# Kernel optimization log

Hardware: AMD Instinct MI355X
Metric: run time of the kernel (lower is better)

The kernel has to match this reference:

```python
import jax, jax.numpy as jnp
import numpy as np

N = 50000      # nodes
C = 16         # input features
NT = 4         # diffusion scales
K1 = 4         # anisotropic kernels
KEIG = 128     # Laplacian eigenpairs
E = 1600000    # edges
HID = 512
OUT = 256


def setup_inputs() -> dict:
    key = jax.random.key(0)
    ks = jax.random.split(key, 10)
    x = jax.random.normal(ks[0], (N, C), dtype=jnp.float32)
    evals = jax.random.uniform(ks[1], (KEIG,), dtype=jnp.float32)
    evecs = jax.random.normal(ks[2], (N, KEIG), dtype=jnp.float32)
    taus = jax.random.uniform(ks[3], (NT,), dtype=jnp.float32)
    kvals = jax.random.normal(ks[4], (K1, E), dtype=jnp.float32)
    edge_index = jax.random.randint(ks[5], (2, E), 0, N, dtype=jnp.int64)
    W1 = jax.random.normal(ks[6], (C * NT * K1, HID), dtype=jnp.float32) * 0.05
    b1 = jnp.zeros((HID,), dtype=jnp.float32)
    W2 = jax.random.normal(ks[7], (HID, OUT), dtype=jnp.float32) * 0.05
    b2 = jnp.zeros((OUT,), dtype=jnp.float32)
    return {"x": x, "evals": evals, "evecs": evecs, "taus": taus,
            "kvals": kvals, "edge_index": edge_index,
            "W1": W1, "b1": b1, "W2": W2, "b2": b2}


def _diffusion(x, evals, evecs, taus):
    # Spectral heat diffusion at NT learned scales, concatenated on channels.
    coeff = evecs.T @ x                                   # [KEIG, C]
    scales = jnp.exp(-evals[None, :] * taus[:, None])      # [NT, KEIG]
    # [N, NT, C] = evecs @ (scale_t * coeff) per scale
    diff = jnp.einsum('nk,tk,kc->ntc', evecs, scales, coeff)
    return diff.reshape(x.shape[0], -1)                    # [N, NT*C]


def _aniso_conv(x, edge_index, kvals):
    # out_k[i] = sum_{edges j->i} K_k[edge] * x[j]; concat over kernels.
    src, dst = edge_index[0], edge_index[1]
    n = x.shape[0]
    outs = []
    for k in range(kvals.shape[0]):  # small fixed loop over K1 kernels
        msgs = kvals[k][:, None] * x[src]                  # [E, NT*C]
        outs.append(jax.ops.segment_sum(msgs, dst, num_segments=n))
    return jnp.concatenate(outs, axis=-1)                  # [N, K1*NT*C]


def reference(x, evals, evecs, taus, kvals, edge_index, W1, b1, W2, b2):
    h = _diffusion(x, evals, evecs, taus)                  # [N, NT*C]
    h = _aniso_conv(h, edge_index, kvals)                  # [N, K1*NT*C]
    h = jax.nn.relu(h @ W1 + b1)                           # MLP layer 1
    h = h @ W2 + b2                                        # MLP layer 2
    # L2 normalize per node (F.normalize with eps=1e-12)
    nrm = jnp.maximum(jnp.linalg.norm(h, axis=-1, keepdims=True), 1e-12)
    return h / nrm
```

## Files before the change

### kernel.cpp

```cpp
#include <hip/hip_runtime.h>

typedef __bf16 bf16_t;
typedef __attribute__((ext_vector_type(8))) __bf16 bf16x8;
typedef __attribute__((ext_vector_type(4))) float f32x4;
typedef unsigned int uint;
typedef unsigned short ushort;
typedef unsigned char uchar;

#define N_NODES 50000
#define C_IN 16
#define NT 4
#define K1 4
#define KEIG 128
#define E_EDGES 1600000
#define HID 512
#define OUT_F 256
#define FEAT 64
#define CONVF 256
#define M_PAD 50048
#define CPB 1024
#define RED1 64
#define SH_C 8
#define NBC 196
#define CAPC 8704
#define PA_B 782

__device__ inline uint bfbits(float f) {
    bf16_t b = (bf16_t)f;
    return (uint)__builtin_bit_cast(unsigned short, b);
}
__device__ inline float bfu(uint u) {
    return __uint_as_float(u << 16);
}

__global__ void coeff_partial_kernel(const float* __restrict__ evecs,
                                     const float* __restrict__ x,
                                     float* __restrict__ partial,
                                     bf16_t* __restrict__ evb, int n) {
    __shared__ float lds[4 * 2048];
    int t = threadIdx.x, lane = t & 63, wid = t >> 6;
    int gw = blockIdx.x * 4 + wid;
    int total_w = gridDim.x * 4;
    int rpw = (n + total_w - 1) / total_w;
    int r0 = gw * rpw;
    int r1 = min(n, r0 + rpw);
    float acc0[16], acc1[16];
#pragma unroll
    for (int c = 0; c < 16; c++) { acc0[c] = 0.f; acc1[c] = 0.f; }
    for (int r = r0; r < r1; r++) {
        float e0 = evecs[(size_t)r * KEIG + lane];
        float e1 = evecs[(size_t)r * KEIG + 64 + lane];
        evb[(size_t)r * KEIG + lane] = (bf16_t)e0;
        evb[(size_t)r * KEIG + 64 + lane] = (bf16_t)e1;
        const float* xr = &x[(size_t)r * C_IN];
#pragma unroll
        for (int c = 0; c < 16; c++) {
            float xv = xr[c];
            acc0[c] += e0 * xv;
            acc1[c] += e1 * xv;
        }
    }
#pragma unroll
    for (int c = 0; c < 16; c++) {
        lds[wid * 2048 + c * 128 + lane] = acc0[c];
        lds[wid * 2048 + c * 128 + 64 + lane] = acc1[c];
    }
    __syncthreads();
    for (int idx = t; idx < 2048; idx += 256) {
        float s = lds[idx] + lds[2048 + idx] + lds[4096 + idx] + lds[6144 + idx];
        partial[(size_t)blockIdx.x * 2048 + idx] = s;
    }
}

__global__ void coeff_reduce1_kernel(const float* __restrict__ partial,
                                     float* __restrict__ partial2) {
    int g = blockIdx.x >> 3;
    int idx = (blockIdx.x & 7) * 256 + threadIdx.x;
    float s = 0.f;
#pragma unroll
    for (int j = 0; j < 16; j++)
        s += partial[(size_t)(g * 16 + j) * 2048 + idx];
    partial2[(size_t)g * 2048 + idx] = s;
}

__global__ void coeff_reduce2_kernel(const float* __restrict__ partial2,
                                     float* __restrict__ coeff) {
    int idx = blockIdx.x * 256 + threadIdx.x;
    float s = 0.f;
#pragma unroll 8
    for (int b = 0; b < RED1; b++) s += partial2[(size_t)b * 2048 + idx];
    coeff[idx] = s;
}

__global__ void sc2t_kernel(const float* __restrict__ evals,
                            const float* __restrict__ taus,
                            const float* __restrict__ coeff,
                            bf16_t* __restrict__ sc2t) {
    int idx = blockIdx.x * 256 + threadIdx.x;
    int col = idx >> 7, k = idx & 127;
    float v = expf(-evals[k] * taus[col >> 4]) * coeff[(col & 15) * 128 + k];
    sc2t[col * KEIG + k] = (bf16_t)v;
}

#define DSTR 136
__global__ void diffusion_mfma_kernel(const bf16_t* __restrict__ evb,
                                      const bf16_t* __restrict__ sc2t,
                                      bf16_t* __restrict__ diffb) {
    __shared__ bf16_t Alds[128 * DSTR];
    __shared__ bf16_t Blds[64 * DSTR];
    const int t = threadIdx.x;
    const int lane = t & 63;
    const int wid = t >> 6;
    const int row0 = blockIdx.x * 128;
#pragma unroll
    for (int i = 0; i < 8; i++) {
        int idx = t + i * 256;
        int r = idx >> 4;
        int k8 = (idx & 15) * 8;
        *(uint4*)&Alds[r * DSTR + k8] =
            *(const uint4*)&evb[(size_t)(row0 + r) * KEIG + k8];
    }
#pragma unroll
    for (int i = 0; i < 4; i++) {
        int idx = t + i * 256;
        int r = idx >> 4;
        int k8 = (idx & 15) * 8;
        *(uint4*)&Blds[r * DSTR + k8] =
            *(const uint4*)&sc2t[r * KEIG + k8];
    }
    __syncthreads();
    f32x4 acc[2][4];
#pragma unroll
    for (int m = 0; m < 2; m++)
#pragma unroll
        for (int n = 0; n < 4; n++) acc[m][n] = (f32x4){0.f, 0.f, 0.f, 0.f};
#pragma unroll
    for (int kk = 0; kk < 128; kk += 32) {
        int ko = kk + ((lane >> 4) << 3);
        bf16x8 av[2], bv[4];
#pragma unroll
        for (int m = 0; m < 2; m++)
            av[m] = *(const bf16x8*)&Alds[(wid * 32 + m * 16 + (lane & 15)) * DSTR + ko];
#pragma unroll
        for (int n = 0; n < 4; n++)
            bv[n] = *(const bf16x8*)&Blds[(n * 16 + (lane & 15)) * DSTR + ko];
#pragma unroll
        for (int m = 0; m < 2; m++)
#pragma unroll
            for (int n = 0; n < 4; n++)
                acc[m][n] = __builtin_amdgcn_mfma_f32_16x16x32_bf16(
                    av[m], bv[n], acc[m][n], 0, 0, 0);
    }
#pragma unroll
    for (int m = 0; m < 2; m++) {
#pragma unroll
        for (int n = 0; n < 4; n++) {
            int col = n * 16 + (lane & 15);
#pragma unroll
            for (int q = 0; q < 4; q++) {
                int row = row0 + wid * 32 + m * 16 + ((lane >> 4) << 2) + q;
                diffb[(size_t)row * FEAT + col] = (bf16_t)acc[m][n][q];
            }
        }
    }
}

__global__ void radixA_kernel(const int* __restrict__ src,
                              const int* __restrict__ dst,
                              const float* __restrict__ kvals,
                              int* __restrict__ gcursor,
                              int4* __restrict__ bucket, int E) {
    __shared__ int hist[256];
    __shared__ int lds_off[256];
    __shared__ int cnt2[256];
    __shared__ int run_base[256];
    __shared__ int4 recs[2048];
    __shared__ uchar posb[2048];
    int t = threadIdx.x;
    hist[t] = 0; cnt2[t] = 0;
    __syncthreads();
    int e0 = blockIdx.x * 2048;
    int total = min(2048, E - e0);
    int d[8];
#pragma unroll
    for (int j = 0; j < 8; j++) {
        int e = e0 + j * 256 + t;
        d[j] = (e < E) ? dst[e] : -1;
        if (d[j] >= 0) atomicAdd(&hist[d[j] >> SH_C], 1);
    }
    __syncthreads();
    int own = hist[t];
    lds_off[t] = own;
    __syncthreads();
    for (int o = 1; o < 256; o <<= 1) {
        int v = (t >= o) ? lds_off[t - o] : 0;
        __syncthreads();
        lds_off[t] += v;
        __syncthreads();
    }
    int excl = lds_off[t] - own;
    __syncthreads();
    lds_off[t] = excl;
    __syncthreads();
#pragma unroll
    for (int j = 0; j < 8; j++) {
        if (d[j] < 0) continue;
        int e = e0 + j * 256 + t;
        int b = d[j] >> SH_C;
        int r = atomicAdd(&cnt2[b], 1);
        int pos = lds_off[b] + r;
        uint w01 = bfbits(kvals[e]) | (bfbits(kvals[(size_t)E + e]) << 16);
        uint w23 = bfbits(kvals[2 * (size_t)E + e]) | (bfbits(kvals[3 * (size_t)E + e]) << 16);
        int4 rec;
        rec.x = src[e]; rec.y = (int)w01; rec.z = (int)w23; rec.w = d[j] & 255;
        recs[pos] = rec;
        posb[pos] = (uchar)b;
    }
    if (t < NBC) {
        int c = hist[t];
        run_base[t] = c ? atomicAdd(&gcursor[t * 16], c) : 0;
    }
    __syncthreads();
    for (int i = t; i < total; i += 256) {
        int b = posb[i];
        int g = run_base[b] + (i - lds_off[b]);
        if (g < CAPC) bucket[(size_t)b * CAPC + g] = recs[i];
    }
}

__global__ void coarse_scan_kernel(const int* __restrict__ gcursor,
                                   int* __restrict__ coarse_base,
                                   int* __restrict__ row_start) {
    __shared__ int lds[256];
    int t = threadIdx.x;
    int own = (t < NBC) ? min(gcursor[t * 16], CAPC) : 0;
    lds[t] = own;
    __syncthreads();
    for (int o = 1; o < 256; o <<= 1) {
        int v = (t >= o) ? lds[t - o] : 0;
        __syncthreads();
        lds[t] += v;
        __syncthreads();
    }
    if (t < NBC) coarse_base[t] = lds[t] - own;
    if (t == 255) row_start[N_NODES] = lds[255];
}

__global__ void radixB_kernel(const int4* __restrict__ bucket,
                              const int* __restrict__ gcursor,
                              const int* __restrict__ coarse_base,
                              int4* __restrict__ csr_rec,
                              int* __restrict__ row_start) {
    __shared__ int hist[256];
    __shared__ int off[256];
    __shared__ int cnt2[256];
    int b = blockIdx.x, t = threadIdx.x;
    int n = min(gcursor[b * 16], CAPC);
    int base = coarse_base[b];
    hist[t] = 0; cnt2[t] = 0;
    __syncthreads();
    const int4* brec = &bucket[(size_t)b * CAPC];
    for (int i = t; i < n; i += 256) atomicAdd(&hist[brec[i].w & 255], 1);
    __syncthreads();
    int own = hist[t];
    off[t] = own;
    __syncthreads();
    for (int o = 1; o < 256; o <<= 1) {
        int v = (t >= o) ? off[t - o] : 0;
        __syncthreads();
        off[t] += v;
        __syncthreads();
    }
    int excl = off[t] - own;
    __syncthreads();
    off[t] = excl;
    __syncthreads();
    int g = b * 256 + t;
    if (g < N_NODES) row_start[g] = base + off[t];
    for (int i = t; i < n; i += 256) {
        int4 rec = brec[i];
        int w = rec.w & 255;
        int r = atomicAdd(&cnt2[w], 1);
        csr_rec[(size_t)(base + off[w] + r)] = rec;
    }
}

__global__ void aniso_kernel(const bf16_t* __restrict__ diffb_,
                             const int* __restrict__ row_start,
                             const int4* __restrict__ csr_rec,
                             bf16_t* __restrict__ conv, int n) {
    const ushort* diffb = (const ushort*)diffb_;
    int wid = (blockIdx.x * 256 + threadIdx.x) >> 6;
    int lane = threadIdx.x & 63;
    if (wid >= n) return;
    int start = __builtin_amdgcn_readfirstlane(row_start[wid]);
    int end = __builtin_amdgcn_readfirstlane(row_start[wid + 1]);
    float a0 = 0.f, a1 = 0.f, a2 = 0.f, a3 = 0.f;
    int p = start;
    for (; p + 8 <= end; p += 8) {
        int s[8];
        uint wy[8], wz[8];
#pragma unroll
        for (int j = 0; j < 8; j++) {
            int4 rec = csr_rec[p + j];
            s[j] = rec.x; wy[j] = (uint)rec.y; wz[j] = (uint)rec.z;
        }
        float h[8];
#pragma unroll
        for (int j = 0; j < 8; j++)
            h[j] = bfu((uint)diffb[(size_t)s[j] * FEAT + lane]);
#pragma unroll
        for (int j = 0; j < 8; j++) {
            a0 += __uint_as_float(wy[j] << 16) * h[j];
            a1 += __uint_as_float(wy[j] & 0xffff0000u) * h[j];
            a2 += __uint_as_float(wz[j] << 16) * h[j];
            a3 += __uint_as_float(wz[j] & 0xffff0000u) * h[j];
        }
    }
    for (; p < end; p++) {
        int4 rec = csr_rec[p];
        float h0 = bfu((uint)diffb[(size_t)rec.x * FEAT + lane]);
        uint y = (uint)rec.y, z = (uint)rec.z;
        a0 += __uint_as_float(y << 16) * h0;
        a1 += __uint_as_float(y & 0xffff0000u) * h0;
        a2 += __uint_as_float(z << 16) * h0;
        a3 += __uint_as_float(z & 0xffff0000u) * h0;
    }
    size_t base = (size_t)wid * CONVF + lane;
    conv[base]       = (bf16_t)a0;
    conv[base + 64]  = (bf16_t)a1;
    conv[base + 128] = (bf16_t)a2;
    conv[base + 192] = (bf16_t)a3;
}

__global__ void convw_kernel(const float* __restrict__ W, bf16_t* __restrict__ Wt,
                             int rows, int cols) {
    int idx = blockIdx.x * 256 + threadIdx.x;
    if (idx >= rows * cols) return;
    int o = idx / rows, f = idx % rows;
    Wt[idx] = (bf16_t)W[(size_t)f * cols + o];
}

#define BM 128
#define BN 128
#define BK 64
#define LSTR 72

template <int EPI>
__global__ void gemm_bf16_kernel(const bf16_t* __restrict__ A,
                                 const bf16_t* __restrict__ Bt,
                                 const float* __restrict__ bias,
                                 void* __restrict__ Cout,
                                 int Nn, int K, int Mvalid) {
    __shared__ bf16_t Alds[BM * LSTR];
    __shared__ bf16_t Blds[BN * LSTR];
    const int t = threadIdx.x;
    const int lane = t & 63;
    const int wid = t >> 6;
    const int row0 = blockIdx.y * BM;
    const int col0 = blockIdx.x * BN;
    const int wr = (wid >> 1) * 64;
    const int wc = (wid & 1) * 64;

    f32x4 acc[4][4];
#pragma unroll
    for (int m = 0; m < 4; m++)
#pragma unroll
        for (int n = 0; n < 4; n++) acc[m][n] = (f32x4){0.f, 0.f, 0.f, 0.f};

    for (int kt = 0; kt < K; kt += BK) {
#pragma unroll
        for (int i = 0; i < 4; i++) {
            int idx = t + i * 256;
            int r = idx >> 3;
            int k8 = (idx & 7) * 8;
            *(uint4*)&Alds[r * LSTR + k8] =
                *(const uint4*)&A[(size_t)(row0 + r) * K + kt + k8];
            *(uint4*)&Blds[r * LSTR + k8] =
                *(const uint4*)&Bt[(size_t)(col0 + r) * K + kt + k8];
        }
        __syncthreads();
#pragma unroll
        for (int kk = 0; kk < BK; kk += 32) {
            int ko = kk + ((lane >> 4) << 3);
            bf16x8 av[4], bv[4];
#pragma unroll
            for (int m = 0; m < 4; m++)
                av[m] = *(const bf16x8*)&Alds[(wr + m * 16 + (lane & 15)) * LSTR + ko];
#pragma unroll
            for (int n = 0; n < 4; n++)
                bv[n] = *(const bf16x8*)&Blds[(wc + n * 16 + (lane & 15)) * LSTR + ko];
#pragma unroll
            for (int m = 0; m < 4; m++)
#pragma unroll
                for (int n = 0; n < 4; n++)
                    acc[m][n] = __builtin_amdgcn_mfma_f32_16x16x32_bf16(
                        av[m], bv[n], acc[m][n], 0, 0, 0);
        }
        __syncthreads();
    }

#pragma unroll
    for (int n = 0; n < 4; n++) {
        int col = col0 + wc + n * 16 + (lane & 15);
        float bvl = bias[col];
#pragma unroll
        for (int m = 0; m < 4; m++) {
#pragma unroll
            for (int r = 0; r < 4; r++) {
                int row = row0 + wr + m * 16 + ((lane >> 4) << 2) + r;
                float v = acc[m][n][r] + bvl;
                if (EPI == 0) {
                    v = v > 0.f ? v : 0.f;
                    ((bf16_t*)Cout)[(size_t)row * Nn + col] = (bf16_t)v;
                } else {
                    if (row < Mvalid)
                        ((float*)Cout)[(size_t)row * Nn + col] = v;
                }
            }
        }
    }
}

__global__ void norm_kernel(float* __restrict__ out, int n) {
    int w = (blockIdx.x * 256 + threadIdx.x) >> 6;
    int lane = threadIdx.x & 63;
    if (w >= n) return;
    float4 v = *(float4*)&out[(size_t)w * OUT_F + lane * 4];
    float ss = v.x * v.x + v.y * v.y + v.z * v.z + v.w * v.w;
#pragma unroll
    for (int off = 32; off > 0; off >>= 1) ss += __shfl_xor(ss, off);
    float nrm = sqrtf(ss);
    nrm = nrm > 1e-12f ? nrm : 1e-12f;
    float sc = 1.f / nrm;
    v.x *= sc; v.y *= sc; v.z *= sc; v.w *= sc;
    *(float4*)&out[(size_t)w * OUT_F + lane * 4] = v;
}

extern "C" void kernel_launch(void* const* d_in, const int* in_sizes, int n_in,
                              void* d_out, int out_size, void* d_ws, size_t ws_size,
                              hipStream_t stream) {
    const float* x      = (const float*)d_in[0];
    const float* evals  = (const float*)d_in[1];
    const float* evecs  = (const float*)d_in[2];
    const float* taus   = (const float*)d_in[3];
    const float* kvals  = (const float*)d_in[4];
    const int*   eidx   = (const int*)d_in[5];
    const float* W1     = (const float*)d_in[6];
    const float* b1     = (const float*)d_in[7];
    const float* W2     = (const float*)d_in[8];
    const float* b2     = (const float*)d_in[9];
    float* out = (float*)d_out;

    const int N = N_NODES, E = E_EDGES;
    const int* e_src = eidx;
    const int* e_dst = eidx + E;

    char* ws = (char*)d_ws;
    size_t off = 0;
    auto alloc = [&](size_t bytes) {
        void* p = ws + off;
        off = (off + bytes + 255) & ~(size_t)255;
        return p;
    };
    float* coeff       = (float*)alloc(2048 * 4);
    float* partial     = (float*)alloc((size_t)CPB * 2048 * 4);
    float* partial2    = (float*)alloc((size_t)RED1 * 2048 * 4);
    bf16_t* evb        = (bf16_t*)alloc((size_t)M_PAD * KEIG * 2);
    bf16_t* sc2t       = (bf16_t*)alloc((size_t)FEAT * KEIG * 2);
    bf16_t* diffb      = (bf16_t*)alloc((size_t)M_PAD * FEAT * 2);
    int*   gcursor     = (int*)alloc((size_t)NBC * 16 * 4);
    int*   coarse_base = (int*)alloc((size_t)(NBC + 1) * 4);
    int*   row_start   = (int*)alloc((size_t)(N + 1) * 4);
    size_t csr_bytes = (size_t)E * 16;
    size_t h1_bytes  = (size_t)M_PAD * HID * 2;
    int4*  csr_rec   = (int4*)alloc(csr_bytes > h1_bytes ? csr_bytes : h1_bytes);
    bf16_t* h1       = (bf16_t*)csr_rec;
    size_t bucket_bytes = (size_t)NBC * CAPC * 16;
    size_t conv_bytes   = (size_t)M_PAD * CONVF * 2;
    int4*  bucket    = (int4*)alloc(bucket_bytes > conv_bytes ? bucket_bytes : conv_bytes);
    bf16_t* conv     = (bf16_t*)bucket;
    bf16_t* w1t      = (bf16_t*)alloc((size_t)HID * CONVF * 2);
    bf16_t* w2t      = (bf16_t*)alloc((size_t)OUT_F * HID * 2);
    (void)ws_size;

    hipMemsetAsync(gcursor, 0, (size_t)NBC * 16 * 4, stream);

    coeff_partial_kernel<<<CPB, 256, 0, stream>>>(evecs, x, partial, evb, N);
    coeff_reduce1_kernel<<<RED1 * 8, 256, 0, stream>>>(partial, partial2);
    coeff_reduce2_kernel<<<8, 256, 0, stream>>>(partial2, coeff);
    sc2t_kernel<<<32, 256, 0, stream>>>(evals, taus, coeff, sc2t);
    diffusion_mfma_kernel<<<M_PAD / 128, 256, 0, stream>>>(evb, sc2t, diffb);

    radixA_kernel<<<PA_B, 256, 0, stream>>>(e_src, e_dst, kvals, gcursor, bucket, E);
    coarse_scan_kernel<<<1, 256, 0, stream>>>(gcursor, coarse_base, row_start);
    radixB_kernel<<<NBC, 256, 0, stream>>>(bucket, gcursor, coarse_base,
                                           csr_rec, row_start);

    aniso_kernel<<<(N + 3) / 4, 256, 0, stream>>>(diffb, row_start, csr_rec, conv, N);

    convw_kernel<<<(CONVF * HID + 255) / 256, 256, 0, stream>>>(W1, w1t, CONVF, HID);
    convw_kernel<<<(HID * OUT_F + 255) / 256, 256, 0, stream>>>(W2, w2t, HID, OUT_F);

    dim3 g1(HID / BN, M_PAD / BM);
    gemm_bf16_kernel<0><<<g1, 256, 0, stream>>>(conv, w1t, b1, h1, HID, CONVF, N);
    dim3 g2(OUT_F / BN, M_PAD / BM);
    gemm_bf16_kernel<1><<<g2, 256, 0, stream>>>(h1, w2t, b2, out, OUT_F, HID, N);

    norm_kernel<<<(N + 3) / 4, 256, 0, stream>>>(out, N);
}
```

Baseline: 219.8 us.

## Fuse second GEMM with L2 row normalization and unroll aniso edge loop

Replaces the second MLP GEMM and separate normalize kernel with one kernel where each block computes 64 full output rows (all 256 columns), reduces squared norms via shuffles and LDS, and writes normalized outputs directly. This removes a full write-then-read of the 50000x256 fp32 output. The aniso gather loop also gains a 16-edge unrolled stage for more memory-level parallelism, at the cost of higher register pressure. The fused GEMM uses a larger per-wave tile (2x8 MFMA accumulators) and a bigger B tile in LDS, which can lower occupancy.

Measured after the change: 235.3 us. +7.0%, slower.

```diff
diff --git a/kernel.cpp b/kernel.cpp
--- a/kernel.cpp
+++ b/kernel.cpp
@@ -297,6 +297,26 @@
     int end = __builtin_amdgcn_readfirstlane(row_start[wid + 1]);
     float a0 = 0.f, a1 = 0.f, a2 = 0.f, a3 = 0.f;
     int p = start;
+    for (; p + 16 <= end; p += 16) {
+        int s[16];
+        uint wy[16], wz[16];
+#pragma unroll
+        for (int j = 0; j < 16; j++) {
+            int4 rec = csr_rec[p + j];
+            s[j] = rec.x; wy[j] = (uint)rec.y; wz[j] = (uint)rec.z;
+        }
+        float h[16];
+#pragma unroll
+        for (int j = 0; j < 16; j++)
+            h[j] = bfu((uint)diffb[(size_t)s[j] * FEAT + lane]);
+#pragma unroll
+        for (int j = 0; j < 16; j++) {
+            a0 += __uint_as_float(wy[j] << 16) * h[j];
+            a1 += __uint_as_float(wy[j] & 0xffff0000u) * h[j];
+            a2 += __uint_as_float(wz[j] << 16) * h[j];
+            a3 += __uint_as_float(wz[j] & 0xffff0000u) * h[j];
+        }
+    }
     for (; p + 8 <= end; p += 8) {
         int s[8];
         uint wy[8], wz[8];
@@ -346,12 +366,11 @@
 #define BK 64
 #define LSTR 72
 
-template <int EPI>
 __global__ void gemm_bf16_kernel(const bf16_t* __restrict__ A,
                                  const bf16_t* __restrict__ Bt,
                                  const float* __restrict__ bias,
-                                 void* __restrict__ Cout,
-                                 int Nn, int K, int Mvalid) {
+                                 bf16_t* __restrict__ Cout,
+                                 int Nn, int K) {
     __shared__ bf16_t Alds[BM * LSTR];
     __shared__ bf16_t Blds[BN * LSTR];
     const int t = threadIdx.x;
@@ -410,31 +429,126 @@
             for (int r = 0; r < 4; r++) {
                 int row = row0 + wr + m * 16 + ((lane >> 4) << 2) + r;
                 float v = acc[m][n][r] + bvl;
-                if (EPI == 0) {
-                    v = v > 0.f ? v : 0.f;
-                    ((bf16_t*)Cout)[(size_t)row * Nn + col] = (bf16_t)v;
-                } else {
-                    if (row < Mvalid)
-                        ((float*)Cout)[(size_t)row * Nn + col] = v;
-                }
+                v = v > 0.f ? v : 0.f;
+                Cout[(size_t)row * Nn + col] = (bf16_t)v;
             }
         }
     }
 }
 
-__global__ void norm_kernel(float* __restrict__ out, int n) {
-    int w = (blockIdx.x * 256 + threadIdx.x) >> 6;
-    int lane = threadIdx.x & 63;
-    if (w >= n) return;
-    float4 v = *(float4*)&out[(size_t)w * OUT_F + lane * 4];
-    float ss = v.x * v.x + v.y * v.y + v.z * v.z + v.w * v.w;
-#pragma unroll
-    for (int off = 32; off > 0; off >>= 1) ss += __shfl_xor(ss, off);
-    float nrm = sqrtf(ss);
-    nrm = nrm > 1e-12f ? nrm : 1e-12f;
-    float sc = 1.f / nrm;
-    v.x *= sc; v.y *= sc; v.z *= sc; v.w *= sc;
-    *(float4*)&out[(size_t)w * OUT_F + lane * 4] = v;
+__global__ void gemm2_norm_kernel(const bf16_t* __restrict__ A,
+                                  const bf16_t* __restrict__ Bt,
+                                  const float* __restrict__ bias,
+                                  float* __restrict__ out, int Mvalid) {
+    __shared__ bf16_t Alds[64 * LSTR];
+    __shared__ bf16_t Blds[256 * LSTR];
+    __shared__ float lds_ss[64 * 2];
+    const int t = threadIdx.x;
+    const int lane = t & 63;
+    const int w = t >> 6;
+    const int row0 = blockIdx.x * 64;
+    const int wr = (w >> 1) * 32;
+    const int wc = (w & 1) * 128;
+    const int K = HID;
+
+    f32x4 acc[2][8];
+#pragma unroll
+    for (int m = 0; m < 2; m++)
+#pragma unroll
+        for (int n = 0; n < 8; n++) acc[m][n] = (f32x4){0.f, 0.f, 0.f, 0.f};
+
+    for (int kt = 0; kt < K; kt += BK) {
+#pragma unroll
+        for (int i = 0; i < 2; i++) {
+            int idx = t + i * 256;
+            int r = idx >> 3;
+            int k8 = (idx & 7) * 8;
+            *(uint4*)&Alds[r * LSTR + k8] =
+                *(const uint4*)&A[(size_t)(row0 + r) * K + kt + k8];
+        }
+#pragma unroll
+        for (int i = 0; i < 8; i++) {
+            int idx = t + i * 256;
+            int r = idx >> 3;
+            int k8 = (idx & 7) * 8;
+            *(uint4*)&Blds[r * LSTR + k8] =
+                *(const uint4*)&Bt[(size_t)r * K + kt + k8];
+        }
+        __syncthreads();
+#pragma unroll
+        for (int kk = 0; kk < BK; kk += 32) {
+            int ko = kk + ((lane >> 4) << 3);
+            bf16x8 av[2], bv[8];
+#pragma unroll
+            for (int m = 0; m < 2; m++)
+                av[m] = *(const bf16x8*)&Alds[(wr + m * 16 + (lane & 15)) * LSTR + ko];
+#pragma unroll
+            for (int n = 0; n < 8; n++)
+                bv[n] = *(const bf16x8*)&Blds[(wc + n * 16 + (lane & 15)) * LSTR + ko];
+#pragma unroll
+            for (int m = 0; m < 2; m++)
+#pragma unroll
+                for (int n = 0; n < 8; n++)
+                    acc[m][n] = __builtin_amdgcn_mfma_f32_16x16x32_bf16(
+                        av[m], bv[n], acc[m][n], 0, 0, 0);
+        }
+        __syncthreads();
+    }
+
+    float ssr[2][4];
+#pragma unroll
+    for (int m = 0; m < 2; m++)
+#pragma unroll
+        for (int q = 0; q < 4; q++) ssr[m][q] = 0.f;
+#pragma unroll
+    for (int n = 0; n < 8; n++) {
+        int col = wc + n * 16 + (lane & 15);
+        float bvl = bias[col];
+#pragma unroll
+        for (int m = 0; m < 2; m++)
+#pragma unroll
+            for (int q = 0; q < 4; q++) {
+                float v = acc[m][n][q] + bvl;
+                ssr[m][q] += v * v;
+            }
+    }
+#pragma unroll
+    for (int m = 0; m < 2; m++)
+#pragma unroll
+        for (int q = 0; q < 4; q++) {
+#pragma unroll
+            for (int o = 1; o < 16; o <<= 1)
+                ssr[m][q] += __shfl_xor(ssr[m][q], o);
+        }
+    if ((lane & 15) == 0) {
+#pragma unroll
+        for (int m = 0; m < 2; m++)
+#pragma unroll
+            for (int q = 0; q < 4; q++) {
+                int rl = wr + m * 16 + ((lane >> 4) << 2) + q;
+                lds_ss[rl * 2 + (w & 1)] = ssr[m][q];
+            }
+    }
+    __syncthreads();
+#pragma unroll
+    for (int m = 0; m < 2; m++) {
+#pragma unroll
+        for (int q = 0; q < 4; q++) {
+            int rl = wr + m * 16 + ((lane >> 4) << 2) + q;
+            int row = row0 + rl;
+            if (row >= Mvalid) continue;
+            float ss = lds_ss[rl * 2] + lds_ss[rl * 2 + 1];
+            float nrm = sqrtf(ss);
+            nrm = nrm > 1e-12f ? nrm : 1e-12f;
+            float sc = 1.f / nrm;
+#pragma unroll
+            for (int n = 0; n < 8; n++) {
+                int col = wc + n * 16 + (lane & 15);
+                float v = acc[m][n][q] + bias[col];
+                out[(size_t)row * OUT_F + col] = v * sc;
+            }
+        }
+    }
 }
 
 extern "C" void kernel_launch(void* const* d_in, const int* in_sizes, int n_in,
@@ -503,9 +617,6 @@
     convw_kernel<<<(HID * OUT_F + 255) / 256, 256, 0, stream>>>(W2, w2t, HID, OUT_F);
 
     dim3 g1(HID / BN, M_PAD / BM);
-    gemm_bf16_kernel<0><<<g1, 256, 0, stream>>>(conv, w1t, b1, h1, HID, CONVF, N);
-    dim3 g2(OUT_F / BN, M_PAD / BM);
-    gemm_bf16_kernel<1><<<g2, 256, 0, stream>>>(h1, w2t, b2, out, OUT_F, HID, N);
-
-    norm_kernel<<<(N + 3) / 4, 256, 0, stream>>>(out, N);
-}
+    gemm_bf16_kernel<<<g1, 256, 0, stream>>>(conv, w1t, b1, h1, HID, CONVF);
+    gemm2_norm_kernel<<<M_PAD / 64, 256, 0, stream>>>(h1, w2t, b2, out, N);
+}
```
